# Kernel optimization log

Hardware: AMD Instinct MI355X
Metric: run time of the kernel (lower is better)

Reference implementation:

```python
import jax, jax.numpy as jnp
import numpy as np

N_QUBITS = 8
N_LAYERS = 2
DIM = 2 ** N_QUBITS  # 256

# ---- 2x2 gate matrices (PennyLane conventions) ----

def _rx(t):
    # RX(t) = [[cos(t/2), -i sin(t/2)], [-i sin(t/2), cos(t/2)]]
    c = jnp.cos(t / 2).astype(jnp.complex64)
    s = (-1j * jnp.sin(t / 2)).astype(jnp.complex64)
    return jnp.stack([jnp.stack([c, s], -1), jnp.stack([s, c], -1)], -2)

def _ry(t):
    c = jnp.cos(t / 2).astype(jnp.complex64)
    s = jnp.sin(t / 2).astype(jnp.complex64)
    return jnp.stack([jnp.stack([c, -s], -1), jnp.stack([s, c], -1)], -2)

def _rz(t):
    e = jnp.exp(-1j * (t / 2).astype(jnp.complex64))
    z = jnp.zeros_like(e)
    return jnp.stack([jnp.stack([e, z], -1), jnp.stack([z, jnp.conj(e)], -1)], -2)

# ---- batched state-vector gate application ----
# state layout: (B, 2, 2, ..., 2); wire 0 is the most-significant axis (PennyLane default.qubit)

def _apply_1q(state, gate, wire):
    ax = 1 + wire
    state = jnp.moveaxis(state, ax, -1)
    if gate.ndim == 2:  # shared gate (trainable weights)
        state = jnp.einsum('...i,ji->...j', state, gate)
    else:               # per-sample gate (angle embedding), gate: (B,2,2)
        state = jnp.einsum('b...i,bji->b...j', state, gate)
    return jnp.moveaxis(state, -1, ax)

def _apply_cnot(state, ctrl, tgt):
    a, b = 1 + ctrl, 1 + tgt
    state = jnp.moveaxis(state, (a, b), (-2, -1))
    # flip target amplitudes where control bit = 1
    state = jnp.concatenate([state[..., 0:1, :], state[..., 1:2, ::-1]], axis=-2)
    return jnp.moveaxis(state, (-2, -1), (a, b))


def _signs():
    idx = np.arange(DIM)
    # bit of wire i in basis index (wire 0 = MSB)
    s = np.stack([1.0 - 2.0 * ((idx >> (N_QUBITS - 1 - i)) & 1)
                  for i in range(N_QUBITS)], axis=1)
    return jnp.asarray(s.astype(np.float32))  # (DIM, N_QUBITS)


def setup_inputs() -> dict:
    key = jax.random.key(0)
    k1, k2 = jax.random.split(key)
    B = 131072
    x = jax.random.normal(k1, (B, N_QUBITS), dtype=jnp.float32)
    weights = jax.random.uniform(k2, (N_LAYERS, N_QUBITS, 3), dtype=jnp.float32,
                                 minval=0.0, maxval=2.0 * np.pi)
    return {"x": x, "weights": weights}


def reference(x, weights):
    B = x.shape[0]
    state = jnp.zeros((B, DIM), jnp.complex64).at[:, 0].set(1.0)
    state = state.reshape((B,) + (2,) * N_QUBITS)
    # AngleEmbedding: RX(x[:, q]) on each wire (default rotation='X')
    for q in range(N_QUBITS):
        state = _apply_1q(state, _rx(x[:, q]), q)
    for l in range(N_LAYERS):
        for q in range(N_QUBITS):
            state = _apply_1q(state, _rx(weights[l, q, 0]), q)
            state = _apply_1q(state, _ry(weights[l, q, 1]), q)
            state = _apply_1q(state, _rz(weights[l, q, 2]), q)
        for q in range(N_QUBITS):
            state = _apply_cnot(state, q, (q + 1) % N_QUBITS)
    probs = jnp.abs(state.reshape(B, DIM)) ** 2  # (B, 256)
    return (probs @ _signs()).astype(jnp.float32)  # <Z_i> per wire, (B, 8)
```

## Files before the change

kernel.cpp:

```cpp
#include <hip/hip_runtime.h>
#include <math.h>


typedef float f2 __attribute__((ext_vector_type(2)));
typedef float f4 __attribute__((ext_vector_type(4)));
typedef _Float16 half4 __attribute__((ext_vector_type(4)));
typedef _Float16 half8 __attribute__((ext_vector_type(8)));

__device__ __forceinline__ f2 cmul_pk(f2 a, f2 b) {
    f2 t, d;
    asm("v_pk_mul_f32 %0, %1, %2 op_sel:[0,0] op_sel_hi:[0,1]"
        : "=v"(t) : "v"(a), "v"(b));
    asm("v_pk_fma_f32 %0, %1, %2, %3 op_sel:[1,1,0] op_sel_hi:[1,0,1] neg_lo:[1,0,0] neg_hi:[0,0,0]"
        : "=v"(d) : "v"(a), "v"(b), "v"(t));
    return d;
}
__device__ __forceinline__ unsigned cmulh(unsigned a, unsigned b) {
    unsigned t, d;
    asm("v_pk_mul_f16 %0, %1, %2 op_sel:[0,0] op_sel_hi:[0,1]"
        : "=v"(t) : "v"(a), "v"(b));
    asm("v_pk_fma_f16 %0, %1, %2, %3 op_sel:[1,1,0] op_sel_hi:[1,0,1] neg_lo:[1,0,0] neg_hi:[0,0,0]"
        : "=v"(d) : "v"(a), "v"(b), "v"(t));
    return d;
}
__device__ __forceinline__ unsigned pkh(f2 v) {
    auto pk = __builtin_amdgcn_cvt_pkrtz(v.x, v.y);
    unsigned u; __builtin_memcpy(&u, &pk, 4);
    return u;
}
__device__ __forceinline__ half4 h4(uint2 u) {
    half4 h; __builtin_memcpy(&h, &u, 8);
    return h;
}
__device__ __forceinline__ f4 mfma16(half4 a, half4 b, f4 c) {
    return __builtin_amdgcn_mfma_f32_16x16x16f16(a, b, c, 0, 0, 0);
}

__global__ void qnn_setup(const float* __restrict__ w, float* __restrict__ p) {
    int t = threadIdx.x;
    if (t < 8) {
        int q = t;
        float cb = cosf(w[q*3+1]*0.5f), sb = sinf(w[q*3+1]*0.5f);
        float cg = cosf(w[q*3+2]*0.5f), sg = sinf(w[q*3+2]*0.5f);
        p[q] = w[q*3+0];
        float* K = p + 8 + q*8;
        K[0] = cg*cb;  K[1] = -sg*cb;
        K[2] = sg*sb;  K[3] = cg*sb;
        K[4] = cg*sb;  K[5] = sg*sb;
        K[6] = sg*cb;  K[7] = -cg*cb;
    }
    float G[8][2][2][2];
    for (int q = 0; q < 8; ++q) {
        const float* wq = w + (8+q)*3;
        float ca = cosf(wq[0]*0.5f), sa = sinf(wq[0]*0.5f);
        float cb = cosf(wq[1]*0.5f), sb = sinf(wq[1]*0.5f);
        float cg = cosf(wq[2]*0.5f), sg = sinf(wq[2]*0.5f);
        float A = cb*ca, Bv = sb*sa, C = sb*ca, D = cb*sa;
        float g00r = cg*A + sg*Bv, g00i = cg*Bv - sg*A;
        float g01r = -(cg*C + sg*D), g01i = sg*C - cg*D;
        G[q][0][0][0]=g00r;  G[q][0][0][1]=g00i;
        G[q][0][1][0]=g01r;  G[q][0][1][1]=g01i;
        G[q][1][0][0]=-g01r; G[q][1][0][1]=g01i;
        G[q][1][1][0]=g00r;  G[q][1][1][1]=-g00i;
    }
    int m = t & 15, k2 = t >> 4;
    float ar = 1.f, ai = 0.f, br = 1.f, bi = 0.f;
    for (int j = 0; j < 4; ++j) {
        int bm = (m >> (3-j)) & 1, bk = (k2 >> (3-j)) & 1;
        float gr = G[j][bm][bk][0],  gi = G[j][bm][bk][1];
        float nr = ar*gr - ai*gi, ni = ar*gi + ai*gr; ar = nr; ai = ni;
        float hr = G[4+j][bm][bk][0], hi = G[4+j][bm][bk][1];
        float mr = br*hr - bi*hi, mi = br*hi + bi*hr; br = mr; bi = mi;
    }
    _Float16* S1Ar  = (_Float16*)((char*)p +  512);
    _Float16* S1Ai  = (_Float16*)((char*)p + 1024);
    _Float16* S1nAi = (_Float16*)((char*)p + 1536);
    _Float16* S2Br  = (_Float16*)((char*)p + 2048);
    _Float16* S2Bi  = (_Float16*)((char*)p + 2560);
    _Float16* S2nBi = (_Float16*)((char*)p + 3072);
    int idx = ((k2 >> 2)*16 + m)*4 + (k2 & 3);
    S1Ar[idx]  = (_Float16)ar;
    S1Ai[idx]  = (_Float16)ai;
    S1nAi[idx] = (_Float16)(-ai);
    S2Br[idx]  = (_Float16)br;
    S2Bi[idx]  = (_Float16)bi;
    S2nBi[idx] = (_Float16)(-bi);

    const int cls[8] = {2, 0, 0, 0, 0, 0, 1, 2};
    const int msk[8] = {55, 12, 14, 15, 47, 63, 63, 63};
    _Float16* SG = (_Float16*)((char*)p + 4608);
    for (int e = t; e < 512; e += 256) {
        int tt = e >> 6, l = e & 63, n = l & 15, quad = l >> 4;
        for (int j = 0; j < 8; ++j) {
            int k  = tt*32 + quad*8 + j;
            int Lp = k >> 2, c = k & 3;
            float v = 0.f;
            if (n < 8 && c == cls[n])
                v = (__popc(msk[n] & Lp) & 1) ? -1.f : 1.f;
            SG[e*8 + j] = (_Float16)v;
        }
    }
}

#define WAVE_LDS 6144

__global__ __launch_bounds__(256, 6) void qnn_main(
        const float* __restrict__ x, const float* __restrict__ p,
        float* __restrict__ out, int B)
{
    __shared__ __align__(16) char smem[4 * WAVE_LDS];
    const int lane = threadIdx.x & 63;
    const int wid  = threadIdx.x >> 6;
    const int L = lane;
    const int b0 = (blockIdx.x * 4 + wid) * 16;
    if (b0 >= B) return;

    char* wb  = smem + wid * WAVE_LDS;
    char* THb = wb;
    char* TCb = wb + 512;
    char* RFb = wb + 2688;
    char* Rb  = wb + 3712;
    f4*   VT  = (f4*)Rb;

    const uint2* ft = (const uint2*)((const char*)p + 512);
    half4 Art  = h4(ft[      L]);
    half4 Ait  = h4(ft[ 64 + L]);
    half4 nAit = h4(ft[128 + L]);
    half4 Brf  = h4(ft[192 + L]);
    half4 Bif  = h4(ft[256 + L]);
    half4 nBif = h4(ft[320 + L]);
    const half8* sgt = (const half8*)((const char*)p + 4608);

    {
        int sI = L >> 2, qp = (L & 3) * 2;
        float2 xv  = ((const float2*)x)[(size_t)(b0 + sI)*4 + (L & 3)];
        float2 w0p = ((const float2*)p)[qp >> 1];
        const f4* Kt = (const f4*)(p + 8);
#pragma unroll
        for (int u = 0; u < 2; ++u) {
            int q = qp + u;
            float ang = (u ? xv.y : xv.x) + (u ? w0p.y : w0p.x);
            float rev = ang * 0.07957747154594767f;
            float ca = __builtin_amdgcn_cosf(rev);
            float sa = __builtin_amdgcn_sinf(rev);
            f4 Ka = Kt[q*2], Kb = Kt[q*2+1];
            f4 v;
            v.x = ca*Ka.x + sa*Ka.z;  v.y = ca*Ka.y + sa*Ka.w;
            v.z = ca*Kb.x + sa*Kb.z;  v.w = ca*Kb.y + sa*Kb.w;
            VT[sI*8 + q] = v;
        }
    }

    {
        int sI = L >> 2, j = L & 3;
        const f4* Vs = VT + sI*8;
        f4 q0v = Vs[0], q1v = Vs[1], q2v = Vs[2], q3v = Vs[3];
        f4 q4v = Vs[4], q5v = Vs[5], q6v = Vs[6], q7v = Vs[7];
        f2 V0a = {q0v.x,q0v.y}, V0b = {q0v.z,q0v.w};
        f2 V1a = {q1v.x,q1v.y}, V1b = {q1v.z,q1v.w};
        f2 V2a = {q2v.x,q2v.y}, V2b = {q2v.z,q2v.w};
        f2 V3a = {q3v.x,q3v.y}, V3b = {q3v.z,q3v.w};
        f2 V4a = {q4v.x,q4v.y}, V4bv = {q4v.z,q4v.w};
        f2 V5a = {q5v.x,q5v.y}, V5b = {q5v.z,q5v.w};
        f2 V6a = {q6v.x,q6v.y}, V6b = {q6v.z,q6v.w};
        f2 V7a = {q7v.x,q7v.y}, V7b = {q7v.z,q7v.w};
        int t1 = j >> 1, t2 = j & 1;
        f2 th0 = cmul_pk(t1 ? V0b : V0a, t2 ? V1b : V1a);
        f2 th1 = cmul_pk(t1 ? V0a : V0b, t2 ? V1a : V1b);
        *(uint2*)(THb + sI*32 + j*8) = (uint2){pkh(th0), pkh(th1)};
        int col3 = j >> 1, col2 = j & 1;
        f2 v5s  = (col3 ^ col2) ? V5b : V5a;
        f2 p6_0 = cmul_pk(v5s, col2 ? V6b : V6a);
        f2 p6_1 = cmul_pk(v5s, col2 ? V6a : V6b);
        f2 V4lo = col3 ? V4bv : V4a;
        f2 V4hi = col3 ? V4a : V4bv;
#pragma unroll
        for (int c = 0; c < 4; ++c) {
            int c1 = c >> 1, c0 = c & 1;
            f2 cf = cmul_pk(c1 ? p6_1 : p6_0, (c1 ^ c0) ? V7b : V7a);
            f2 e0 = cmul_pk(cf, V4lo);
            f2 e1 = cmul_pk(cf, V4hi);
            *(uint2*)(TCb + sI*136 + (4*j + c)*8) = (uint2){pkh(e0), pkh(e1)};
        }
        unsigned rr[4];
#pragma unroll
        for (int r = 0; r < 4; ++r) {
            int r1 = r >> 1, r0 = r & 1;
            f2 rf = cmul_pk(((j & 1) ^ r1) ? V2b : V2a, (r1 ^ r0) ? V3b : V3a);
            rr[r] = pkh(rf);
        }
        *(uint4*)(RFb + sI*64 + j*16) = (uint4){rr[0], rr[1], rr[2], rr[3]};
    }

    const int hq  = L >> 4;
    const int col = L & 15;
    const int th_t1 = hq >> 1, th_t2 = (hq >> 1) ^ (hq & 1);
    char* THl = THb + ((th_t1*2 + th_t2)*2 + (col & 1))*4;
    char* TCl = TCb + col*8;
    char* RFl = RFb + hq*16;
    char* Rw  = Rb + L*8;
    char* Rr  = Rb + (col & 3)*544 + hq*16;
    const f4 zz = {0.f, 0.f, 0.f, 0.f};

    for (int h = 0; h < 4; ++h) {
#pragma unroll
        for (int s4 = 0; s4 < 4; ++s4) {
            const int s = h*4 + s4;
            unsigned u  = *(const unsigned*)(THl + s*32);
            uint2   tc  = *(const uint2*)(TCl + s*136);
            uint4   rf  = *(const uint4*)(RFl + s*64);
            unsigned g0 = cmulh(u, tc.x);
            unsigned g1 = cmulh(u, tc.y);
            unsigned a0 = cmulh(rf.x, g0);
            unsigned a1 = cmulh(rf.y, g1);
            unsigned a2 = cmulh(rf.z, g0);
            unsigned a3 = cmulh(rf.w, g1);
            half4 Srf = h4((uint2){ __builtin_amdgcn_perm(a1, a0, 0x05040100u),
                                    __builtin_amdgcn_perm(a3, a2, 0x05040100u) });
            half4 Sif = h4((uint2){ __builtin_amdgcn_perm(a1, a0, 0x07060302u),
                                    __builtin_amdgcn_perm(a3, a2, 0x07060302u) });
            f4 Tr4 = mfma16(Sif, nAit, mfma16(Srf, Art, zz));
            f4 Ti4 = mfma16(Sif, Art,  mfma16(Srf, Ait, zz));
            half4 Trf = h4((uint2){ pkh((f2){Tr4[0], Tr4[1]}),
                                    pkh((f2){Tr4[2], Tr4[3]}) });
            half4 Tif = h4((uint2){ pkh((f2){Ti4[0], Ti4[1]}),
                                    pkh((f2){Ti4[2], Ti4[3]}) });
            f4 Pr4 = mfma16(nBif, Tif, mfma16(Brf, Trf, zz));
            f4 Pi4 = mfma16(Bif,  Trf, mfma16(Brf, Tif, zz));
            float Q0 = Pr4[0]*Pr4[0] + Pi4[0]*Pi4[0];
            float Q1 = Pr4[1]*Pr4[1] + Pi4[1]*Pi4[1];
            float Q2 = Pr4[2]*Pr4[2] + Pi4[2]*Pi4[2];
            float Q3 = Pr4[3]*Pr4[3] + Pi4[3]*Pi4[3];
            float s01 = Q0 + Q1, s23 = Q2 + Q3;
            float S00 = s01 + s23;
            float S10 = s01 - s23;
            float S11 = (Q0 - Q1) - (Q2 - Q3);
            uint2 wv = { pkh((f2){S00, S10}), pkh((f2){S11, 0.f}) };
            *(uint2*)(Rw + s4*544) = wv;
        }
        f4 acc = zz;
#pragma unroll
        for (int tt = 0; tt < 8; ++tt) {
            uint4 rv = *(uint4*)(Rr + tt*64);
            half8 af;
            __builtin_memcpy(&af, &rv, 16);
            acc = __builtin_amdgcn_mfma_f32_16x16x32_f16(af, sgt[tt*64 + L], acc, 0, 0, 0);
        }
        if (hq == 0 && col < 8) {
            size_t base = (size_t)(b0 + h*4) * 8 + col;
            out[base     ] = acc[0];
            out[base +  8] = acc[1];
            out[base + 16] = acc[2];
            out[base + 24] = acc[3];
        }
    }
}

extern "C" void kernel_launch(void* const* d_in, const int* in_sizes, int n_in,
                              void* d_out, int out_size, void* d_ws, size_t ws_size,
                              hipStream_t stream) {
    const float* x = (const float*)d_in[0];
    const float* w = (const float*)d_in[1];
    float* outp    = (float*)d_out;
    float* params  = (float*)d_ws;
    int B = in_sizes[0] / 8;

    qnn_setup<<<1, 256, 0, stream>>>(w, params);
    int blocks = (B + 63) / 64;
    qnn_main<<<blocks, 256, 0, stream>>>(x, params, outp, B);
}
```

Before: 83.74 us.

## Fold setup kernel into main kernel and bake sign table at compile time

Removes the separate single-block setup launch. Each wave now recomputes the layer-2 gate fragments and the layer-1 RY/RZ coefficients from the raw weights using hardware sin/cos. The constant sign table becomes a compile-time device array. This drops a kernel launch and its serialization gap, but every wave repeats the trig and complex-product work, which also adds register pressure.

```diff
diff --git a/kernel.cpp b/kernel.cpp
--- a/kernel.cpp
+++ b/kernel.cpp
@@ -36,76 +36,37 @@
     return __builtin_amdgcn_mfma_f32_16x16x16f16(a, b, c, 0, 0, 0);
 }
 
-__global__ void qnn_setup(const float* __restrict__ w, float* __restrict__ p) {
-    int t = threadIdx.x;
-    if (t < 8) {
-        int q = t;
-        float cb = cosf(w[q*3+1]*0.5f), sb = sinf(w[q*3+1]*0.5f);
-        float cg = cosf(w[q*3+2]*0.5f), sg = sinf(w[q*3+2]*0.5f);
-        p[q] = w[q*3+0];
-        float* K = p + 8 + q*8;
-        K[0] = cg*cb;  K[1] = -sg*cb;
-        K[2] = sg*sb;  K[3] = cg*sb;
-        K[4] = cg*sb;  K[5] = sg*sb;
-        K[6] = sg*cb;  K[7] = -cg*cb;
-    }
-    float G[8][2][2][2];
-    for (int q = 0; q < 8; ++q) {
-        const float* wq = w + (8+q)*3;
-        float ca = cosf(wq[0]*0.5f), sa = sinf(wq[0]*0.5f);
-        float cb = cosf(wq[1]*0.5f), sb = sinf(wq[1]*0.5f);
-        float cg = cosf(wq[2]*0.5f), sg = sinf(wq[2]*0.5f);
-        float A = cb*ca, Bv = sb*sa, C = sb*ca, D = cb*sa;
-        float g00r = cg*A + sg*Bv, g00i = cg*Bv - sg*A;
-        float g01r = -(cg*C + sg*D), g01i = sg*C - cg*D;
-        G[q][0][0][0]=g00r;  G[q][0][0][1]=g00i;
-        G[q][0][1][0]=g01r;  G[q][0][1][1]=g01i;
-        G[q][1][0][0]=-g01r; G[q][1][0][1]=g01i;
-        G[q][1][1][0]=g00r;  G[q][1][1][1]=-g00i;
-    }
-    int m = t & 15, k2 = t >> 4;
-    float ar = 1.f, ai = 0.f, br = 1.f, bi = 0.f;
-    for (int j = 0; j < 4; ++j) {
-        int bm = (m >> (3-j)) & 1, bk = (k2 >> (3-j)) & 1;
-        float gr = G[j][bm][bk][0],  gi = G[j][bm][bk][1];
-        float nr = ar*gr - ai*gi, ni = ar*gi + ai*gr; ar = nr; ai = ni;
-        float hr = G[4+j][bm][bk][0], hi = G[4+j][bm][bk][1];
-        float mr = br*hr - bi*hi, mi = br*hi + bi*hr; br = mr; bi = mi;
-    }
-    _Float16* S1Ar  = (_Float16*)((char*)p +  512);
-    _Float16* S1Ai  = (_Float16*)((char*)p + 1024);
-    _Float16* S1nAi = (_Float16*)((char*)p + 1536);
-    _Float16* S2Br  = (_Float16*)((char*)p + 2048);
-    _Float16* S2Bi  = (_Float16*)((char*)p + 2560);
-    _Float16* S2nBi = (_Float16*)((char*)p + 3072);
-    int idx = ((k2 >> 2)*16 + m)*4 + (k2 & 3);
-    S1Ar[idx]  = (_Float16)ar;
-    S1Ai[idx]  = (_Float16)ai;
-    S1nAi[idx] = (_Float16)(-ai);
-    S2Br[idx]  = (_Float16)br;
-    S2Bi[idx]  = (_Float16)bi;
-    S2nBi[idx] = (_Float16)(-bi);
-
+__device__ __forceinline__ f2 gsel(const float* g, int r, int c) {
+    f2 e0 = c ? (f2){g[2],  g[3]} : (f2){ g[0], g[1]};
+    f2 e1 = c ? (f2){g[0], -g[1]} : (f2){-g[2], g[3]};
+    return r ? e1 : e0;
+}
+
+struct SgTab { unsigned short v[4096]; };
+constexpr int cpop(int x) { int c = 0; while (x) { c += x & 1; x >>= 1; } return c; }
+constexpr SgTab make_sg() {
+    SgTab t{};
     const int cls[8] = {2, 0, 0, 0, 0, 0, 1, 2};
     const int msk[8] = {55, 12, 14, 15, 47, 63, 63, 63};
-    _Float16* SG = (_Float16*)((char*)p + 4608);
-    for (int e = t; e < 512; e += 256) {
+    for (int e = 0; e < 512; ++e) {
         int tt = e >> 6, l = e & 63, n = l & 15, quad = l >> 4;
         for (int j = 0; j < 8; ++j) {
-            int k  = tt*32 + quad*8 + j;
+            int k = tt*32 + quad*8 + j;
             int Lp = k >> 2, c = k & 3;
-            float v = 0.f;
+            unsigned short hv = 0;
             if (n < 8 && c == cls[n])
-                v = (__popc(msk[n] & Lp) & 1) ? -1.f : 1.f;
-            SG[e*8 + j] = (_Float16)v;
-        }
-    }
-}
+                hv = (cpop(msk[n] & Lp) & 1) ? 0xBC00 : 0x3C00;
+            t.v[e*8 + j] = hv;
+        }
+    }
+    return t;
+}
+__device__ constexpr SgTab SG = make_sg();
 
 #define WAVE_LDS 6144
 
 __global__ __launch_bounds__(256, 6) void qnn_main(
-        const float* __restrict__ x, const float* __restrict__ p,
+        const float* __restrict__ x, const float* __restrict__ w,
         float* __restrict__ out, int B)
 {
     __shared__ __align__(16) char smem[4 * WAVE_LDS];
@@ -122,31 +83,65 @@
     char* Rb  = wb + 3712;
     f4*   VT  = (f4*)Rb;
 
-    const uint2* ft = (const uint2*)((const char*)p + 512);
-    half4 Art  = h4(ft[      L]);
-    half4 Ait  = h4(ft[ 64 + L]);
-    half4 nAit = h4(ft[128 + L]);
-    half4 Brf  = h4(ft[192 + L]);
-    half4 Bif  = h4(ft[256 + L]);
-    half4 nBif = h4(ft[320 + L]);
-    const half8* sgt = (const half8*)((const char*)p + 4608);
+    const float CREV = 0.07957747154594767f;
+    const int hq  = L >> 4;
+    const int col = L & 15;
+
+    half4 Art, Ait, nAit, Brf, Bif, nBif;
+    {
+        const int mb0 = (col>>3)&1, mb1 = (col>>2)&1, mb2 = (col>>1)&1, mb3 = col&1;
+        const int q1 = (hq>>1)&1, q0 = hq&1;
+        float gv[4][4];
+#pragma unroll
+        for (int half = 0; half < 2; ++half) {
+#pragma unroll
+            for (int q = 0; q < 4; ++q) {
+                const float* wq = w + (8 + half*4 + q)*3;
+                float ra = wq[0]*CREV, rb = wq[1]*CREV, rg = wq[2]*CREV;
+                float ca = __builtin_amdgcn_cosf(ra), sa = __builtin_amdgcn_sinf(ra);
+                float cb = __builtin_amdgcn_cosf(rb), sb = __builtin_amdgcn_sinf(rb);
+                float cg = __builtin_amdgcn_cosf(rg), sg = __builtin_amdgcn_sinf(rg);
+                float A = cb*ca, Bv = sb*sa, Cc = sb*ca, D = cb*sa;
+                gv[q][0] = cg*A + sg*Bv;
+                gv[q][1] = cg*Bv - sg*A;
+                gv[q][2] = -(cg*Cc + sg*D);
+                gv[q][3] = sg*Cc - cg*D;
+            }
+            f2 P01 = cmul_pk(gsel(gv[0], mb0, q1), gsel(gv[1], mb1, q0));
+            f2 Xj[4];
+#pragma unroll
+            for (int j = 0; j < 4; ++j)
+                Xj[j] = cmul_pk(P01, cmul_pk(gsel(gv[2], mb2, j>>1),
+                                             gsel(gv[3], mb3, j&1)));
+            half4 Xr = h4((uint2){ pkh((f2){Xj[0].x, Xj[1].x}),
+                                   pkh((f2){Xj[2].x, Xj[3].x}) });
+            half4 Xi = h4((uint2){ pkh((f2){Xj[0].y, Xj[1].y}),
+                                   pkh((f2){Xj[2].y, Xj[3].y}) });
+            half4 Xn = h4((uint2){ pkh((f2){-Xj[0].y, -Xj[1].y}),
+                                   pkh((f2){-Xj[2].y, -Xj[3].y}) });
+            if (half == 0) { Art = Xr; Ait = Xi; nAit = Xn; }
+            else           { Brf = Xr; Bif = Xi; nBif = Xn; }
+        }
+    }
+    const half8* sgt = (const half8*)SG.v;
 
     {
         int sI = L >> 2, qp = (L & 3) * 2;
-        float2 xv  = ((const float2*)x)[(size_t)(b0 + sI)*4 + (L & 3)];
-        float2 w0p = ((const float2*)p)[qp >> 1];
-        const f4* Kt = (const f4*)(p + 8);
+        float2 xv = ((const float2*)x)[(size_t)(b0 + sI)*4 + (L & 3)];
 #pragma unroll
         for (int u = 0; u < 2; ++u) {
             int q = qp + u;
-            float ang = (u ? xv.y : xv.x) + (u ? w0p.y : w0p.x);
-            float rev = ang * 0.07957747154594767f;
-            float ca = __builtin_amdgcn_cosf(rev);
-            float sa = __builtin_amdgcn_sinf(rev);
-            f4 Ka = Kt[q*2], Kb = Kt[q*2+1];
+            float w0 = w[q*3+0], w1 = w[q*3+1], w2 = w[q*3+2];
+            float ang = (u ? xv.y : xv.x) + w0;
+            float ra = ang * CREV, rb = w1 * CREV, rg = w2 * CREV;
+            float ca = __builtin_amdgcn_cosf(ra), sa = __builtin_amdgcn_sinf(ra);
+            float cb = __builtin_amdgcn_cosf(rb), sb = __builtin_amdgcn_sinf(rb);
+            float cg = __builtin_amdgcn_cosf(rg), sg = __builtin_amdgcn_sinf(rg);
             f4 v;
-            v.x = ca*Ka.x + sa*Ka.z;  v.y = ca*Ka.y + sa*Ka.w;
-            v.z = ca*Kb.x + sa*Kb.z;  v.w = ca*Kb.y + sa*Kb.w;
+            v.x = ca*(cg*cb) + sa*(sg*sb);
+            v.y = sa*(cg*sb) - ca*(sg*cb);
+            v.z = ca*(cg*sb) + sa*(sg*cb);
+            v.w = ca*(sg*sb) - sa*(cg*cb);
             VT[sI*8 + q] = v;
         }
     }
@@ -192,8 +187,6 @@
         *(uint4*)(RFb + sI*64 + j*16) = (uint4){rr[0], rr[1], rr[2], rr[3]};
     }
 
-    const int hq  = L >> 4;
-    const int col = L & 15;
     const int th_t1 = hq >> 1, th_t2 = (hq >> 1) ^ (hq & 1);
     char* THl = THb + ((th_t1*2 + th_t2)*2 + (col & 1))*4;
     char* TCl = TCb + col*8;
@@ -262,10 +255,8 @@
     const float* x = (const float*)d_in[0];
     const float* w = (const float*)d_in[1];
     float* outp    = (float*)d_out;
-    float* params  = (float*)d_ws;
     int B = in_sizes[0] / 8;
 
-    qnn_setup<<<1, 256, 0, stream>>>(w, params);
     int blocks = (B + 63) / 64;
-    qnn_main<<<blocks, 256, 0, stream>>>(x, params, outp, B);
-}
+    qnn_main<<<blocks, 256, 0, stream>>>(x, w, outp, B);
+}
```

Measured after the change: 80.17 us. 1.04x faster.
